# Performance work log

Measured on AMD Instinct MI355X. Metric: run time of the kernel, lower is better.

## Reference

```python
import jax, jax.numpy as jnp
import numpy as np

B, L, D, H, K = 8, 200, 256, 8, 20
HS = D // H


def setup_inputs() -> dict:
    key = jax.random.key(0)
    ks = jax.random.split(key, 12)
    def xavier(k, shape):
        fan_in, fan_out = shape[1], shape[0]
        lim = np.sqrt(2.0) * np.sqrt(6.0 / (fan_in + fan_out))  # gain=relu
        return jax.random.uniform(k, shape, jnp.float32, -lim, lim)
    return {
        "seqs": jax.random.normal(ks[0], (B, L, D), jnp.float32),
        "attention_mask": jax.random.bernoulli(ks[1], 0.3, (L, L)),
        "time_matrices": jax.random.normal(ks[2], (B, L, L, D), jnp.float32),
        "conv1_w": xavier(ks[3], (D, D)),
        "conv1_b": jnp.zeros((D,), jnp.float32),
        "conv2_w": xavier(ks[4], (D, D)),
        "conv2_b": jnp.zeros((D,), jnp.float32),
        "W_w": jax.random.normal(ks[5], (D, D), jnp.float32) * (1.0 / np.sqrt(D)),
        "W_b": jnp.zeros((D,), jnp.float32),
        "ln_gamma": jnp.ones((D,), jnp.float32),
        "ln_beta": jnp.zeros((D,), jnp.float32),
    }


def _to_heads(x):
    # torch.cat(torch.split(x, HS, dim=-1), dim=0): [B,L,D] -> [H*B,L,HS], index h*B+b
    return jnp.concatenate(jnp.split(x, H, axis=-1), axis=0)


def _from_heads(x):
    # inverse: [H*B,L,HS] -> [B,L,D]
    return jnp.concatenate(jnp.split(x, H, axis=0), axis=-1)


def reference(seqs, attention_mask, time_matrices, conv1_w, conv1_b,
              conv2_w, conv2_b, W_w, W_b, ln_gamma, ln_beta):
    # 1x1 Conv1d == per-token linear
    a_ = seqs @ conv1_w.T + conv1_b
    b_ = seqs @ conv2_w.T + conv2_b
    a = _to_heads(a_)                    # [HB, L, HS]
    b = _to_heads(b_)                    # [HB, L, HS]
    ti = jnp.concatenate(jnp.split(time_matrices, H, axis=3), axis=0)  # [HB, L, L, HS]

    # attention scores: QK^T + time interaction
    att = jnp.einsum('bqh,bkh->bqk', a, b) + jnp.einsum('bqkh,bqh->bqk', ti, a)
    a_2 = jnp.linalg.norm(a, axis=-1)[..., None]              # [HB, L, 1]
    b_t_2 = jnp.linalg.norm(b[:, None, :, :] + ti, axis=-1)   # [HB, L, L]
    raw_graph = att / (a_2 * b_t_2 + 1e-6)

    attn_mask = jnp.broadcast_to(attention_mask[None], raw_graph.shape)
    raw_graph = jnp.where(attn_mask, 0.0, raw_graph)

    # top-K per row, symmetric binary mask (vectorized scatter)
    _, idx = jax.lax.top_k(raw_graph, K)                      # [HB, L, K]
    HB = raw_graph.shape[0]
    bi = jnp.arange(HB)[:, None, None]
    ri = jnp.arange(L)[None, :, None]
    mask = jnp.zeros_like(raw_graph).at[bi, ri, idx].set(1.0)
    mask = mask.at[bi, idx, ri].set(1.0)
    mask = jax.lax.stop_gradient(mask)

    sparse_graph = jnp.where(attn_mask, 0.0, raw_graph * mask)

    seqs_h = _to_heads(seqs @ W_w.T + W_b)                    # [HB, L, HS]
    outputs = sparse_graph @ seqs_h                           # [HB, L, HS]
    time_outputs = jnp.einsum('bqk,bqkh->bqh', sparse_graph, ti)

    outputs = _from_heads(outputs)                            # [B, L, D]
    time_outputs = _from_heads(time_outputs)                  # [B, L, D]

    # LayerNorm(eps=1e-8), biased variance (torch semantics)
    mu = outputs.mean(-1, keepdims=True)
    var = ((outputs - mu) ** 2).mean(-1, keepdims=True)
    ln = (outputs - mu) / jnp.sqrt(var + 1e-8) * ln_gamma + ln_beta
    return ln, time_outputs
```

## Files before the change

### kernel.cpp

```cpp
#include <hip/hip_runtime.h>
#include <hip/hip_bf16.h>

#define B_  8
#define L_  200
#define D_  256
#define H_  8
#define HS_ 32
#define K_  20
#define BL_ 1600
#define G_  64
#define MW_ 7
#define NEG_INF (-3.402823466e38f)

__device__ __forceinline__ float bf2f(unsigned short u){
  return __uint_as_float(((unsigned int)u) << 16);
}
__device__ __forceinline__ unsigned short f2bf(float f){
  unsigned int x = __float_as_uint(f);
  unsigned int r = (x + 0x7fffu + ((x >> 16) & 1u)) >> 16;
  return (unsigned short)r;
}
__device__ __forceinline__ void up2(unsigned int u, float& lo, float& hi){
  lo = __uint_as_float(u << 16);
  hi = __uint_as_float(u & 0xffff0000u);
}

__device__ __forceinline__ float loadf(const void* base, size_t i, int fp){
  return fp ? ((const float*)base)[i] : bf2f(((const unsigned short*)base)[i]);
}
__device__ __forceinline__ void load8f(const void* base, size_t i, int fp, float f[8]){
  if (fp){
    const float4* p = (const float4*)((const float*)base + i);
    float4 x = p[0], y = p[1];
    f[0]=x.x; f[1]=x.y; f[2]=x.z; f[3]=x.w; f[4]=y.x; f[5]=y.y; f[6]=y.z; f[7]=y.w;
  } else {
    uint4 v = *(const uint4*)((const unsigned short*)base + i);
    up2(v.x,f[0],f[1]); up2(v.y,f[2],f[3]); up2(v.z,f[4],f[5]); up2(v.w,f[6],f[7]);
  }
}
__device__ __forceinline__ int mask_at(const void* am, int i, int mk){
  switch(mk){
    case 0:  return ((const int*)am)[i] != 0;
    case 1:  return ((const unsigned char*)am)[i] != 0;
    case 2:  return ((const unsigned int*)am)[i] != 0;
    default: return ((const unsigned short*)am)[i] != 0;
  }
}
__device__ __forceinline__ void storef(void* base, size_t i, int fp, float v){
  if (fp) ((float*)base)[i] = v; else ((unsigned short*)base)[i] = f2bf(v);
}

__global__ __launch_bounds__(256) void k_detect(
    const unsigned short* __restrict__ seqs, const unsigned int* __restrict__ am,
    int* __restrict__ flags)
{
  int t = threadIdx.x;
  __shared__ int r[5];
  if (t < 5) r[t] = 0;
  __syncthreads();

  int bad = 0;
  for (int i = t; i < 4096; i += 256){
    unsigned e = (seqs[i] >> 7) & 0xFFu;
    if (e >= 160u) bad++;
  }
  int vi = 0, vb = 0, vf = 0, vh = 0;
  for (int i = t; i < 1024; i += 256){
    unsigned w = am[i];
    if (w == 0u) continue;
    if (w == 1u) vi++;
    else if (w == 0x3F800000u) vf++;
    else if (w == 0x00003F80u || w == 0x3F803F80u) vh++;
    else if ((w & 0xFEFEFEFEu) == 0u) vb++;
    else vb++;
  }
  atomicAdd(&r[0], bad); atomicAdd(&r[1], vi); atomicAdd(&r[2], vb);
  atomicAdd(&r[3], vf);  atomicAdd(&r[4], vh);
  __syncthreads();
  if (t == 0){
    flags[0] = (r[0] > 32) ? 1 : 0;
    int kind;
    if (r[2] > r[1] && r[2] > r[3] + r[4]) kind = 1;
    else if (r[4] > 0)                     kind = 3;
    else if (r[3] > r[1])                  kind = 2;
    else                                   kind = 0;
    flags[1] = kind;
  }
}

__global__ __launch_bounds__(256) void kz_zero(unsigned int* __restrict__ p, int n){
  int i = blockIdx.x * 256 + threadIdx.x;
  if (i < n) p[i] = 0u;
}

__global__ __launch_bounds__(256) void k1_linear(
    const void* __restrict__ seqs,
    const void* __restrict__ w1, const void* __restrict__ b1,
    const void* __restrict__ w2, const void* __restrict__ b2,
    const void* __restrict__ w3, const void* __restrict__ b3,
    const int* __restrict__ flags,
    float* __restrict__ da, float* __restrict__ db, float* __restrict__ dsh)
{
  int fp = flags[0];
  int bid = blockIdx.x;
  int m  = bid / 400;
  int rb = (bid % 400) * 4;
  const void* w; const void* bias; float* dst;
  if (m == 0)      { w = w1; bias = b1; dst = da;  }
  else if (m == 1) { w = w2; bias = b2; dst = db;  }
  else             { w = w3; bias = b3; dst = dsh; }

  __shared__ float s4[4][D_];
  int t = threadIdx.x;
  for (int l = t; l < 4 * D_; l += 256){
    int rr = l >> 8, c = l & 255;
    s4[rr][c] = loadf(seqs, (size_t)(rb + rr) * D_ + c, fp);
  }
  __syncthreads();

  float acc[4];
  float bv = loadf(bias, t, fp);
  #pragma unroll
  for (int rr = 0; rr < 4; rr++) acc[rr] = bv;

  for (int c8 = 0; c8 < 32; c8++){
    float wf[8];
    load8f(w, (size_t)t * D_ + c8 * 8, fp, wf);
    #pragma unroll
    for (int rr = 0; rr < 4; rr++){
      const float* sf = &s4[rr][c8 * 8];
      #pragma unroll
      for (int i = 0; i < 8; i++) acc[rr] += sf[i] * wf[i];
    }
  }
  #pragma unroll
  for (int rr = 0; rr < 4; rr++)
    dst[(size_t)(rb + rr) * D_ + t] = acc[rr];
}

__global__ __launch_bounds__(256) void k2_rawtopk(
    const float* __restrict__ a_, const float* __restrict__ b_,
    const void* __restrict__ tm, const void* __restrict__ am,
    const int* __restrict__ flags, unsigned int* __restrict__ maskw,
    float* __restrict__ rawg)
{
  int fp = flags[0], mk = flags[1];
  int bid = blockIdx.x;
  int bb = bid / L_;
  int q  = bid - bb * L_;
  int t = threadIdx.x;
  int rsub = t >> 5;
  int cg   = t & 31;
  int c0   = cg * 8;
  int h    = cg >> 2;

  __shared__ float raw_sh[8 * 208];

  float areg[8];
  const float* arow = a_ + (size_t)(bb * L_ + q) * D_;
  {
    const float4* a4 = (const float4*)(arow + c0);
    float4 x = a4[0], y = a4[1];
    areg[0]=x.x; areg[1]=x.y; areg[2]=x.z; areg[3]=x.w;
    areg[4]=y.x; areg[5]=y.y; areg[6]=y.z; areg[7]=y.w;
  }
  float a2;
  {
    float s = 0.f;
    #pragma unroll
    for (int e = 0; e < 8; e++) s += areg[e] * areg[e];
    s += __shfl_xor(s, 1);
    s += __shfl_xor(s, 2);
    a2 = sqrtf(s);
  }

  const size_t tmbase = (size_t)(bb * L_ + q) * L_ * D_;
  const float* bbase  = b_ + (size_t)bb * L_ * D_;
  const int amrow = q * L_;

  for (int k0 = 0; k0 < L_; k0 += 8){
    int k = k0 + rsub;
    float tf[8];
    load8f(tm, tmbase + (size_t)k * D_ + c0, fp, tf);
    const float4* b4 = (const float4*)(bbase + (size_t)k * D_ + c0);
    float4 bv0 = b4[0], bv1 = b4[1];
    float bf[8] = {bv0.x, bv0.y, bv0.z, bv0.w, bv1.x, bv1.y, bv1.z, bv1.w};
    float p1 = 0.f, p2 = 0.f;
    #pragma unroll
    for (int i = 0; i < 8; i++){
      float sv = bf[i] + tf[i];
      p1 += areg[i] * sv;
      p2 += sv * sv;
    }
    p1 += __shfl_xor(p1, 1); p2 += __shfl_xor(p2, 1);
    p1 += __shfl_xor(p1, 2); p2 += __shfl_xor(p2, 2);
    if ((cg & 3) == 0){
      float r = p1 / (a2 * sqrtf(p2) + 1e-6f);
      if (mask_at(am, amrow + k, mk)) r = 0.f;
      raw_sh[h * 208 + k] = r;
    }
  }
  __syncthreads();

  if (rawg){
    #pragma unroll
    for (int hh2 = 0; hh2 < 8; hh2++){
      if (t < L_)
        rawg[((size_t)(hh2 * B_ + bb) * L_ + q) * L_ + t] = raw_sh[hh2 * 208 + t];
    }
  }

  int wv = t >> 6, lane = t & 63;
  for (int hh = 2 * wv; hh <= 2 * wv + 1; hh++){
    const float* r = &raw_sh[hh * 208];
    int g = hh * B_ + bb;

    float v0 = (lane       < L_) ? r[lane]       : NEG_INF;
    float v1 = (lane + 64  < L_) ? r[lane + 64]  : NEG_INF;
    float v2 = (lane + 128 < L_) ? r[lane + 128] : NEG_INF;
    float v3 = (lane + 192 < L_) ? r[lane + 192] : NEG_INF;

    for (int it = 0; it < K_; it++){
      float bv = v0; int bi = lane;
      if (v1 > bv){ bv = v1; bi = lane + 64;  }
      if (v2 > bv){ bv = v2; bi = lane + 128; }
      if (v3 > bv){ bv = v3; bi = lane + 192; }
      #pragma unroll
      for (int off = 1; off < 64; off <<= 1){
        float ov = __shfl_xor(bv, off);
        int   oi = __shfl_xor(bi, off);
        if (ov > bv || (ov == bv && oi < bi)){ bv = ov; bi = oi; }
      }
      if (bi == lane)            v0 = NEG_INF;
      else if (bi == lane + 64)  v1 = NEG_INF;
      else if (bi == lane + 128) v2 = NEG_INF;
      else if (bi == lane + 192) v3 = NEG_INF;
      if (lane == 0){
        atomicOr(&maskw[((size_t)g * L_ + q)  * MW_ + (bi >> 5)], 1u << (bi & 31));
        atomicOr(&maskw[((size_t)g * L_ + bi) * MW_ + (q  >> 5)], 1u << (q  & 31));
      }
    }
  }
}

__global__ __launch_bounds__(256) void k3_gatherln(
    const float* __restrict__ a_, const float* __restrict__ b_,
    const float* __restrict__ sh_, const void* __restrict__ tm,
    const void* __restrict__ am, const unsigned int* __restrict__ maskw,
    const void* __restrict__ gamma, const void* __restrict__ beta,
    const int* __restrict__ flags, const float* __restrict__ rawg,
    void* __restrict__ out)
{
  int fp = flags[0], mk = flags[1];
  int bid = blockIdx.x;
  int bb = bid / L_;
  int q  = bid - bb * L_;
  int t = threadIdx.x;

  __shared__ float a_sh[D_];
  __shared__ float s_a2[8];
  __shared__ int   s_k[8][200];
  __shared__ float s_v[8][200];
  __shared__ int   s_cnt[8];
  __shared__ float red[8];

  a_sh[t] = a_[(size_t)(bb * L_ + q) * D_ + t];
  __syncthreads();
  if (t < 8){
    float s = 0.f;
    #pragma unroll
    for (int e = 0; e < HS_; e++){ float d = a_sh[t * HS_ + e]; s += d * d; }
    s_a2[t] = sqrtf(s);
  }
  __syncthreads();

  int wv = t >> 6, lane = t & 63;
  for (int hh = 2 * wv; hh <= 2 * wv + 1; hh++){
    int g = hh * B_ + bb;
    const unsigned int* mrow = &maskw[((size_t)g * L_ + q) * MW_];
    int cnt = 0;
    #pragma unroll
    for (int c = 0; c < 4; c++){
      int k = c * 64 + lane;
      bool sel = (k < L_) && ((mrow[k >> 5] >> (k & 31)) & 1u) && !mask_at(am, q * L_ + k, mk);
      unsigned long long bal = __ballot(sel);
      int pos = __popcll(bal & ((1ull << lane) - 1ull));
      if (sel) s_k[hh][cnt + pos] = k;
      cnt += __popcll(bal);
    }
    if (lane == 0) s_cnt[hh] = cnt;

    if (rawg){
      const float* rrow = rawg + ((size_t)g * L_ + q) * L_;
      for (int i = lane; i < cnt; i += 64)
        s_v[hh][i] = rrow[s_k[hh][i]];
    } else {
      float a2 = s_a2[hh];
      for (int i = lane; i < cnt; i += 64){
        int k = s_k[hh][i];
        size_t pbase = ((size_t)(bb * L_ + q) * L_ + k) * D_ + hh * HS_;
        const float4* b4 = (const float4*)(b_ + (size_t)(bb * L_ + k) * D_ + hh * HS_);
        float p1 = 0.f, p2 = 0.f;
        #pragma unroll
        for (int e8 = 0; e8 < 4; e8++){
          float tf[8];
          load8f(tm, pbase + e8 * 8, fp, tf);
          float4 bv0 = b4[e8 * 2], bv1 = b4[e8 * 2 + 1];
          float bf[8] = {bv0.x, bv0.y, bv0.z, bv0.w, bv1.x, bv1.y, bv1.z, bv1.w};
          #pragma unroll
          for (int i2 = 0; i2 < 8; i2++){
            float s = bf[i2] + tf[i2];
            p1 += a_sh[hh * HS_ + e8 * 8 + i2] * s;
            p2 += s * s;
          }
        }
        s_v[hh][i] = p1 / (a2 * sqrtf(p2) + 1e-6f);
      }
    }
  }
  __syncthreads();

  int h = t >> 5, hs = t & 31;
  int cnt = s_cnt[h];
  float acc_o = 0.f, acc_t = 0.f;
  const size_t tmrow = (size_t)(bb * L_ + q) * L_ * D_;
  for (int i = 0; i < cnt; i++){
    int k = s_k[h][i];
    float v = s_v[h][i];
    acc_o += v * sh_[(size_t)(bb * L_ + k) * D_ + h * HS_ + hs];
    acc_t += v * loadf(tm, tmrow + (size_t)k * D_ + h * HS_ + hs, fp);
  }
  size_t orow = (size_t)(bb * L_ + q) * D_;
  storef(out, (size_t)409600 + orow + t, fp, acc_t);

  float s = acc_o;
  #pragma unroll
  for (int off = 1; off < 64; off <<= 1) s += __shfl_xor(s, off);
  if (lane == 0) red[wv] = s;
  __syncthreads();
  float mean = (red[0] + red[1] + red[2] + red[3]) * (1.f / 256.f);

  float d = acc_o - mean;
  float s2 = d * d;
  #pragma unroll
  for (int off = 1; off < 64; off <<= 1) s2 += __shfl_xor(s2, off);
  if (lane == 0) red[4 + wv] = s2;
  __syncthreads();
  float var = (red[4] + red[5] + red[6] + red[7]) * (1.f / 256.f);

  float y = d * (1.f / sqrtf(var + 1e-8f)) * loadf(gamma, t, fp) + loadf(beta, t, fp);
  storef(out, orow + t, fp, y);
}

extern "C" void kernel_launch(void* const* d_in, const int* in_sizes, int n_in,
                              void* d_out, int out_size, void* d_ws, size_t ws_size,
                              hipStream_t stream) {
  const void* seqs = d_in[0];
  const void* am   = d_in[1];
  const void* tm   = d_in[2];
  const void* w1   = d_in[3];
  const void* b1   = d_in[4];
  const void* w2   = d_in[5];
  const void* b2   = d_in[6];
  const void* w3   = d_in[7];
  const void* b3   = d_in[8];
  const void* lng  = d_in[9];
  const void* lnb  = d_in[10];

  float* ws = (float*)d_ws;
  int*   flags = (int*)ws;
  float* a_    = ws + 16;
  float* b_    = ws + 16 + 409600;
  float* sh_   = ws + 16 + 819200;
  unsigned int* maskw = (unsigned int*)(ws + 16 + 1228800);
  float* rawg  = ws + 16 + 1228800 + 89600;
  size_t need  = ((size_t)16 + 1228800 + 89600 + 2560000) * 4;
  float* rawg_arg = (ws_size >= need) ? rawg : nullptr;

  k_detect   <<<1,   256, 0, stream>>>((const unsigned short*)seqs, (const unsigned int*)am, flags);
  kz_zero    <<<350, 256, 0, stream>>>(maskw, G_ * L_ * MW_);
  k1_linear  <<<1200, 256, 0, stream>>>(seqs, w1, b1, w2, b2, w3, b3, flags, a_, b_, sh_);
  k2_rawtopk <<<BL_, 256, 0, stream>>>(a_, b_, tm, am, flags, maskw, rawg_arg);
  k3_gatherln<<<BL_, 256, 0, stream>>>(a_, b_, sh_, tm, am, maskw, lng, lnb, flags, rawg_arg, d_out);
}
```

Baseline: 610.3 us.

## Split top-k into separate row-parallel kernel and merge init kernels

Moves top-K selection out of the raw-score kernel into its own kernel where each wavefront handles one row (3200 blocks), so score computation no longer stalls on serial top-k loops. Merges the detect and zero kernels into one launch, unrolls the score loop by two, and unrolls the gather loop with dual accumulators to keep more loads in flight. The rawg workspace buffer becomes mandatory: the fallback path that recomputed scores when the workspace was too small is removed, which fails if the workspace is undersized.

```diff
diff --git a/kernel.cpp b/kernel.cpp
--- a/kernel.cpp
+++ b/kernel.cpp
@@ -50,47 +50,47 @@
   if (fp) ((float*)base)[i] = v; else ((unsigned short*)base)[i] = f2bf(v);
 }
 
-__global__ __launch_bounds__(256) void k_detect(
+__global__ __launch_bounds__(256) void k0_init(
     const unsigned short* __restrict__ seqs, const unsigned int* __restrict__ am,
-    int* __restrict__ flags)
+    int* __restrict__ flags, unsigned int* __restrict__ maskw)
 {
   int t = threadIdx.x;
-  __shared__ int r[5];
-  if (t < 5) r[t] = 0;
-  __syncthreads();
-
-  int bad = 0;
-  for (int i = t; i < 4096; i += 256){
-    unsigned e = (seqs[i] >> 7) & 0xFFu;
-    if (e >= 160u) bad++;
-  }
-  int vi = 0, vb = 0, vf = 0, vh = 0;
-  for (int i = t; i < 1024; i += 256){
-    unsigned w = am[i];
-    if (w == 0u) continue;
-    if (w == 1u) vi++;
-    else if (w == 0x3F800000u) vf++;
-    else if (w == 0x00003F80u || w == 0x3F803F80u) vh++;
-    else if ((w & 0xFEFEFEFEu) == 0u) vb++;
-    else vb++;
-  }
-  atomicAdd(&r[0], bad); atomicAdd(&r[1], vi); atomicAdd(&r[2], vb);
-  atomicAdd(&r[3], vf);  atomicAdd(&r[4], vh);
-  __syncthreads();
-  if (t == 0){
-    flags[0] = (r[0] > 32) ? 1 : 0;
-    int kind;
-    if (r[2] > r[1] && r[2] > r[3] + r[4]) kind = 1;
-    else if (r[4] > 0)                     kind = 3;
-    else if (r[3] > r[1])                  kind = 2;
-    else                                   kind = 0;
-    flags[1] = kind;
-  }
-}
-
-__global__ __launch_bounds__(256) void kz_zero(unsigned int* __restrict__ p, int n){
-  int i = blockIdx.x * 256 + threadIdx.x;
-  if (i < n) p[i] = 0u;
+  int i = blockIdx.x * 256 + t;
+  if (i < G_ * L_ * MW_) maskw[i] = 0u;
+
+  if (blockIdx.x == 350){
+    __shared__ int r[5];
+    if (t < 5) r[t] = 0;
+    __syncthreads();
+
+    int bad = 0;
+    for (int j = t; j < 4096; j += 256){
+      unsigned e = (seqs[j] >> 7) & 0xFFu;
+      if (e >= 160u) bad++;
+    }
+    int vi = 0, vb = 0, vf = 0, vh = 0;
+    for (int j = t; j < 1024; j += 256){
+      unsigned w = am[j];
+      if (w == 0u) continue;
+      if (w == 1u) vi++;
+      else if (w == 0x3F800000u) vf++;
+      else if (w == 0x00003F80u || w == 0x3F803F80u) vh++;
+      else if ((w & 0xFEFEFEFEu) == 0u) vb++;
+      else vb++;
+    }
+    atomicAdd(&r[0], bad); atomicAdd(&r[1], vi); atomicAdd(&r[2], vb);
+    atomicAdd(&r[3], vf);  atomicAdd(&r[4], vh);
+    __syncthreads();
+    if (t == 0){
+      flags[0] = (r[0] > 32) ? 1 : 0;
+      int kind;
+      if (r[2] > r[1] && r[2] > r[3] + r[4]) kind = 1;
+      else if (r[4] > 0)                     kind = 3;
+      else if (r[3] > r[1])                  kind = 2;
+      else                                   kind = 0;
+      flags[1] = kind;
+    }
+  }
 }
 
 __global__ __launch_bounds__(256) void k1_linear(
@@ -138,11 +138,10 @@
     dst[(size_t)(rb + rr) * D_ + t] = acc[rr];
 }
 
-__global__ __launch_bounds__(256) void k2_rawtopk(
+__global__ __launch_bounds__(256) void k2a_raw(
     const float* __restrict__ a_, const float* __restrict__ b_,
     const void* __restrict__ tm, const void* __restrict__ am,
-    const int* __restrict__ flags, unsigned int* __restrict__ maskw,
-    float* __restrict__ rawg)
+    const int* __restrict__ flags, float* __restrict__ rawg)
 {
   int fp = flags[0], mk = flags[1];
   int bid = blockIdx.x;
@@ -178,6 +177,7 @@
   const float* bbase  = b_ + (size_t)bb * L_ * D_;
   const int amrow = q * L_;
 
+  #pragma unroll 2
   for (int k0 = 0; k0 < L_; k0 += 8){
     int k = k0 + rsub;
     float tf[8];
@@ -202,54 +202,55 @@
   }
   __syncthreads();
 
-  if (rawg){
-    #pragma unroll
-    for (int hh2 = 0; hh2 < 8; hh2++){
-      if (t < L_)
-        rawg[((size_t)(hh2 * B_ + bb) * L_ + q) * L_ + t] = raw_sh[hh2 * 208 + t];
-    }
-  }
-
-  int wv = t >> 6, lane = t & 63;
-  for (int hh = 2 * wv; hh <= 2 * wv + 1; hh++){
-    const float* r = &raw_sh[hh * 208];
-    int g = hh * B_ + bb;
-
-    float v0 = (lane       < L_) ? r[lane]       : NEG_INF;
-    float v1 = (lane + 64  < L_) ? r[lane + 64]  : NEG_INF;
-    float v2 = (lane + 128 < L_) ? r[lane + 128] : NEG_INF;
-    float v3 = (lane + 192 < L_) ? r[lane + 192] : NEG_INF;
-
-    for (int it = 0; it < K_; it++){
-      float bv = v0; int bi = lane;
-      if (v1 > bv){ bv = v1; bi = lane + 64;  }
-      if (v2 > bv){ bv = v2; bi = lane + 128; }
-      if (v3 > bv){ bv = v3; bi = lane + 192; }
-      #pragma unroll
-      for (int off = 1; off < 64; off <<= 1){
-        float ov = __shfl_xor(bv, off);
-        int   oi = __shfl_xor(bi, off);
-        if (ov > bv || (ov == bv && oi < bi)){ bv = ov; bi = oi; }
-      }
-      if (bi == lane)            v0 = NEG_INF;
-      else if (bi == lane + 64)  v1 = NEG_INF;
-      else if (bi == lane + 128) v2 = NEG_INF;
-      else if (bi == lane + 192) v3 = NEG_INF;
-      if (lane == 0){
-        atomicOr(&maskw[((size_t)g * L_ + q)  * MW_ + (bi >> 5)], 1u << (bi & 31));
-        atomicOr(&maskw[((size_t)g * L_ + bi) * MW_ + (q  >> 5)], 1u << (q  & 31));
-      }
+  #pragma unroll
+  for (int hh2 = 0; hh2 < 8; hh2++){
+    if (t < L_)
+      rawg[((size_t)(hh2 * B_ + bb) * L_ + q) * L_ + t] = raw_sh[hh2 * 208 + t];
+  }
+}
+
+__global__ __launch_bounds__(256) void k2b_topk(
+    const float* __restrict__ rawg, unsigned int* __restrict__ maskw)
+{
+  int wv = threadIdx.x >> 6, lane = threadIdx.x & 63;
+  int row = blockIdx.x * 4 + wv;
+  int g = row / L_;
+  int q = row - g * L_;
+  const float* r = rawg + (size_t)row * L_;
+
+  float v0 = r[lane];
+  float v1 = r[lane + 64];
+  float v2 = (lane + 128 < L_) ? r[lane + 128] : NEG_INF;
+  float v3 = (lane + 192 < L_) ? r[lane + 192] : NEG_INF;
+
+  for (int it = 0; it < K_; it++){
+    float bv = v0; int bi = lane;
+    if (v1 > bv){ bv = v1; bi = lane + 64;  }
+    if (v2 > bv){ bv = v2; bi = lane + 128; }
+    if (v3 > bv){ bv = v3; bi = lane + 192; }
+    #pragma unroll
+    for (int off = 1; off < 64; off <<= 1){
+      float ov = __shfl_xor(bv, off);
+      int   oi = __shfl_xor(bi, off);
+      if (ov > bv || (ov == bv && oi < bi)){ bv = ov; bi = oi; }
+    }
+    if (bi == lane)            v0 = NEG_INF;
+    else if (bi == lane + 64)  v1 = NEG_INF;
+    else if (bi == lane + 128) v2 = NEG_INF;
+    else if (bi == lane + 192) v3 = NEG_INF;
+    if (lane == 0){
+      atomicOr(&maskw[((size_t)g * L_ + q)  * MW_ + (bi >> 5)], 1u << (bi & 31));
+      atomicOr(&maskw[((size_t)g * L_ + bi) * MW_ + (q  >> 5)], 1u << (q  & 31));
     }
   }
 }
 
 __global__ __launch_bounds__(256) void k3_gatherln(
-    const float* __restrict__ a_, const float* __restrict__ b_,
     const float* __restrict__ sh_, const void* __restrict__ tm,
     const void* __restrict__ am, const unsigned int* __restrict__ maskw,
+    const float* __restrict__ rawg,
     const void* __restrict__ gamma, const void* __restrict__ beta,
-    const int* __restrict__ flags, const float* __restrict__ rawg,
-    void* __restrict__ out)
+    const int* __restrict__ flags, void* __restrict__ out)
 {
   int fp = flags[0], mk = flags[1];
   int bid = blockIdx.x;
@@ -257,22 +258,10 @@
   int q  = bid - bb * L_;
   int t = threadIdx.x;
 
-  __shared__ float a_sh[D_];
-  __shared__ float s_a2[8];
   __shared__ int   s_k[8][200];
   __shared__ float s_v[8][200];
   __shared__ int   s_cnt[8];
   __shared__ float red[8];
-
-  a_sh[t] = a_[(size_t)(bb * L_ + q) * D_ + t];
-  __syncthreads();
-  if (t < 8){
-    float s = 0.f;
-    #pragma unroll
-    for (int e = 0; e < HS_; e++){ float d = a_sh[t * HS_ + e]; s += d * d; }
-    s_a2[t] = sqrtf(s);
-  }
-  __syncthreads();
 
   int wv = t >> 6, lane = t & 63;
   for (int hh = 2 * wv; hh <= 2 * wv + 1; hh++){
@@ -290,46 +279,38 @@
     }
     if (lane == 0) s_cnt[hh] = cnt;
 
-    if (rawg){
-      const float* rrow = rawg + ((size_t)g * L_ + q) * L_;
-      for (int i = lane; i < cnt; i += 64)
-        s_v[hh][i] = rrow[s_k[hh][i]];
-    } else {
-      float a2 = s_a2[hh];
-      for (int i = lane; i < cnt; i += 64){
-        int k = s_k[hh][i];
-        size_t pbase = ((size_t)(bb * L_ + q) * L_ + k) * D_ + hh * HS_;
-        const float4* b4 = (const float4*)(b_ + (size_t)(bb * L_ + k) * D_ + hh * HS_);
-        float p1 = 0.f, p2 = 0.f;
-        #pragma unroll
-        for (int e8 = 0; e8 < 4; e8++){
-          float tf[8];
-          load8f(tm, pbase + e8 * 8, fp, tf);
-          float4 bv0 = b4[e8 * 2], bv1 = b4[e8 * 2 + 1];
-          float bf[8] = {bv0.x, bv0.y, bv0.z, bv0.w, bv1.x, bv1.y, bv1.z, bv1.w};
-          #pragma unroll
-          for (int i2 = 0; i2 < 8; i2++){
-            float s = bf[i2] + tf[i2];
-            p1 += a_sh[hh * HS_ + e8 * 8 + i2] * s;
-            p2 += s * s;
-          }
-        }
-        s_v[hh][i] = p1 / (a2 * sqrtf(p2) + 1e-6f);
-      }
-    }
+    const float* rrow = rawg + ((size_t)g * L_ + q) * L_;
+    for (int i = lane; i < cnt; i += 64)
+      s_v[hh][i] = rrow[s_k[hh][i]];
   }
   __syncthreads();
 
   int h = t >> 5, hs = t & 31;
+  int hb = h * HS_ + hs;
   int cnt = s_cnt[h];
-  float acc_o = 0.f, acc_t = 0.f;
   const size_t tmrow = (size_t)(bb * L_ + q) * L_ * D_;
-  for (int i = 0; i < cnt; i++){
-    int k = s_k[h][i];
-    float v = s_v[h][i];
-    acc_o += v * sh_[(size_t)(bb * L_ + k) * D_ + h * HS_ + hs];
-    acc_t += v * loadf(tm, tmrow + (size_t)k * D_ + h * HS_ + hs, fp);
-  }
+  const float* shb = sh_ + (size_t)bb * L_ * D_;
+
+  float acc_o = 0.f, acc_t = 0.f, acc_o1 = 0.f, acc_t1 = 0.f;
+  int i = 0;
+  for (; i + 2 <= cnt; i += 2){
+    int ka = s_k[h][i], kb = s_k[h][i + 1];
+    float va = s_v[h][i], vb = s_v[h][i + 1];
+    float soa = shb[(size_t)ka * D_ + hb];
+    float sob = shb[(size_t)kb * D_ + hb];
+    float sta = loadf(tm, tmrow + (size_t)ka * D_ + hb, fp);
+    float stb = loadf(tm, tmrow + (size_t)kb * D_ + hb, fp);
+    acc_o  += va * soa;  acc_t  += va * sta;
+    acc_o1 += vb * sob;  acc_t1 += vb * stb;
+  }
+  if (i < cnt){
+    int ka = s_k[h][i];
+    float va = s_v[h][i];
+    acc_o += va * shb[(size_t)ka * D_ + hb];
+    acc_t += va * loadf(tm, tmrow + (size_t)ka * D_ + hb, fp);
+  }
+  acc_o += acc_o1;  acc_t += acc_t1;
+
   size_t orow = (size_t)(bb * L_ + q) * D_;
   storef(out, (size_t)409600 + orow + t, fp, acc_t);
 
@@ -374,12 +355,10 @@
   float* sh_   = ws + 16 + 819200;
   unsigned int* maskw = (unsigned int*)(ws + 16 + 1228800);
   float* rawg  = ws + 16 + 1228800 + 89600;
-  size_t need  = ((size_t)16 + 1228800 + 89600 + 2560000) * 4;
-  float* rawg_arg = (ws_size >= need) ? rawg : nullptr;
-
-  k_detect   <<<1,   256, 0, stream>>>((const unsigned short*)seqs, (const unsigned int*)am, flags);
-  kz_zero    <<<350, 256, 0, stream>>>(maskw, G_ * L_ * MW_);
+
+  k0_init    <<<351,  256, 0, stream>>>((const unsigned short*)seqs, (const unsigned int*)am, flags, maskw);
   k1_linear  <<<1200, 256, 0, stream>>>(seqs, w1, b1, w2, b2, w3, b3, flags, a_, b_, sh_);
-  k2_rawtopk <<<BL_, 256, 0, stream>>>(a_, b_, tm, am, flags, maskw, rawg_arg);
-  k3_gatherln<<<BL_, 256, 0, stream>>>(a_, b_, sh_, tm, am, maskw, lng, lnb, flags, rawg_arg, d_out);
-}
+  k2a_raw    <<<BL_,  256, 0, stream>>>(a_, b_, tm, am, flags, rawg);
+  k2b_topk   <<<3200, 256, 0, stream>>>(rawg, maskw);
+  k3_gatherln<<<BL_,  256, 0, stream>>>(sh_, tm, am, maskw, rawg, lng, lnb, flags, d_out);
+}
```

Measured after the change: 586.6 us. 3.9% less time.
